# Kernel optimization log

Measured on AMD Instinct MI355X. Metric: run time of the kernel, lower is better.

The kernel has to match this reference:

```python
import jax, jax.numpy as jnp
import numpy as np

EPS = 1e-5

def layernorm(x, w, b):
    mu = jnp.mean(x, axis=-1, keepdims=True)
    xc = x - mu
    var = jnp.mean(xc * xc, axis=-1, keepdims=True)
    return xc * jax.lax.rsqrt(var + EPS) * w + b

def setup_inputs() -> dict:
    key = jax.random.key(0)
    ks = jax.random.split(key, 9)
    B, T, Nm, Nl = 8, 8, 1024, 64
    Vw, Tw, H, Dh = 1024, 2048, 8, 64
    inner = H * Dh  # 512
    s_q = 1.0 / np.sqrt(Tw)
    s_kv = 1.0 / np.sqrt(Vw)
    s_o = 1.0 / np.sqrt(inner)
    return {
        "x": jax.random.normal(ks[0], (B, T, Nm, Vw), jnp.float32),
        "latents": jax.random.normal(ks[1], (B, T, Nl, Tw), jnp.float32),
        "nm_w": jnp.ones((Vw,), jnp.float32),
        "nm_b": jnp.zeros((Vw,), jnp.float32),
        "nl_w": jnp.ones((Tw,), jnp.float32),
        "nl_b": jnp.zeros((Tw,), jnp.float32),
        "Wq": jax.random.normal(ks[2], (Tw, inner), jnp.float32) * s_q,
        "Wkv": jax.random.normal(ks[3], (Vw, 2 * inner), jnp.float32) * s_kv,
        "Wout": jax.random.normal(ks[4], (inner, Tw), jnp.float32) * s_o,
    }

def reference(x, latents, nm_w, nm_b, nl_w, nl_b, Wq, Wkv, Wout):
    H, Dh = 8, 64
    scale = Dh ** (-0.5)
    B, T, Nm, _ = x.shape
    Nl = latents.shape[2]
    xn = layernorm(x, nm_w, nm_b)          # (B,T,Nm,Vw)
    ln = layernorm(latents, nl_w, nl_b)    # (B,T,Nl,Tw)
    q = (ln @ Wq).reshape(B, T, Nl, H, Dh)           # b t i h d
    kv = xn @ Wkv                                     # (B,T,Nm,2*inner)
    k, v = jnp.split(kv, 2, axis=-1)
    k = k.reshape(B, T, Nm, H, Dh)                    # b t j h d
    v = v.reshape(B, T, Nm, H, Dh)
    sim = jnp.einsum('btihd,btjhd->bthij', q * scale, k)  # (B,T,H,Nl,Nm)
    attn = jax.nn.softmax(sim, axis=-1)
    out = jnp.einsum('bthij,btjhd->btihd', attn, v)       # (B,T,Nl,H,Dh)
    out = out.reshape(B, T, Nl, H * Dh)
    return out @ Wout                                     # (B,T,Nl,Tw)
```

## Files before the change

### kernel.cpp

```cpp
#include <hip/hip_runtime.h>

typedef __attribute__((ext_vector_type(8))) short bfrag8;
typedef __attribute__((ext_vector_type(4))) float f32x4;

typedef const unsigned int __attribute__((address_space(1)))* gas1_u32;
typedef unsigned int __attribute__((address_space(3)))* gas3_u32;

#define DEV __device__ __forceinline__

DEV unsigned short f2bf(float f) {
  unsigned int u = __builtin_bit_cast(unsigned int, f);
  u += 0x7fffu + ((u >> 16) & 1u);
  return (unsigned short)(u >> 16);
}

DEV void gload_lds16(const void* g, void* l) {
  __builtin_amdgcn_global_load_lds((gas1_u32)g, (gas3_u32)l, 16, 0, 0);
}

__global__ __launch_bounds__(256) void k_pre(
    const float* __restrict__ x, unsigned short* __restrict__ xb,
    float* __restrict__ mu, float* __restrict__ rstd,
    const float* __restrict__ lat, const float* __restrict__ nl_w,
    const float* __restrict__ nl_b, unsigned short* __restrict__ lnb,
    const float* __restrict__ Wq,   unsigned short* __restrict__ WqT,
    const float* __restrict__ Wkv,  unsigned short* __restrict__ WkvT,
    const float* __restrict__ Wout, unsigned short* __restrict__ WoutT,
    const float* __restrict__ nm_w, const float* __restrict__ nm_b,
    float* __restrict__ part)
{
  __shared__ float smem[32 * 33];
  const int bid = blockIdx.x, tid = threadIdx.x;
  const int wid = tid >> 6, lane = tid & 63;

  if (bid < 16384) {
    const int row = bid * 4 + wid;
    const float* base = x + (size_t)row * 1024;
    float4 v[4];
    #pragma unroll
    for (int i = 0; i < 4; ++i) v[i] = ((const float4*)base)[i * 64 + lane];
    float s = 0.f, q = 0.f;
    #pragma unroll
    for (int i = 0; i < 4; ++i) {
      s += v[i].x + v[i].y + v[i].z + v[i].w;
      q += v[i].x*v[i].x + v[i].y*v[i].y + v[i].z*v[i].z + v[i].w*v[i].w;
    }
    #pragma unroll
    for (int off = 32; off >= 1; off >>= 1) { s += __shfl_xor(s, off); q += __shfl_xor(q, off); }
    const float m  = s * (1.0f/1024.0f);
    const float var = q * (1.0f/1024.0f) - m * m;
    const float rs = rsqrtf(var + 1e-5f);
    if (lane == 0) { mu[row] = m; rstd[row] = rs; }
    unsigned short* ob = xb + (size_t)row * 1024;
    #pragma unroll
    for (int i = 0; i < 4; ++i) {
      ushort4 o;
      o.x = f2bf(v[i].x); o.y = f2bf(v[i].y); o.z = f2bf(v[i].z); o.w = f2bf(v[i].w);
      ((ushort4*)ob)[i * 64 + lane] = o;
    }
    return;
  }
  if (bid < 20480) {
    const int row = bid - 16384;
    const float* base = lat + (size_t)row * 2048;
    const float4 v0 = ((const float4*)base)[tid];
    const float4 v1 = ((const float4*)base)[256 + tid];
    float s = v0.x+v0.y+v0.z+v0.w + v1.x+v1.y+v1.z+v1.w;
    float q = v0.x*v0.x+v0.y*v0.y+v0.z*v0.z+v0.w*v0.w
            + v1.x*v1.x+v1.y*v1.y+v1.z*v1.z+v1.w*v1.w;
    #pragma unroll
    for (int off = 32; off >= 1; off >>= 1) { s += __shfl_xor(s, off); q += __shfl_xor(q, off); }
    if (lane == 0) { smem[wid] = s; smem[4 + wid] = q; }
    __syncthreads();
    s = smem[0] + smem[1] + smem[2] + smem[3];
    q = smem[4] + smem[5] + smem[6] + smem[7];
    const float m  = s * (1.0f/2048.0f);
    const float var = q * (1.0f/2048.0f) - m * m;
    const float rs = rsqrtf(var + 1e-5f);
    const float4 w0 = ((const float4*)nl_w)[tid], w1 = ((const float4*)nl_w)[256 + tid];
    const float4 b0 = ((const float4*)nl_b)[tid], b1 = ((const float4*)nl_b)[256 + tid];
    ushort4 o0, o1;
    o0.x = f2bf((v0.x - m) * rs * w0.x + b0.x);
    o0.y = f2bf((v0.y - m) * rs * w0.y + b0.y);
    o0.z = f2bf((v0.z - m) * rs * w0.z + b0.z);
    o0.w = f2bf((v0.w - m) * rs * w0.w + b0.w);
    o1.x = f2bf((v1.x - m) * rs * w1.x + b1.x);
    o1.y = f2bf((v1.y - m) * rs * w1.y + b1.y);
    o1.z = f2bf((v1.z - m) * rs * w1.z + b1.z);
    o1.w = f2bf((v1.w - m) * rs * w1.w + b1.w);
    ((ushort4*)(lnb + (size_t)row * 2048))[tid] = o0;
    ((ushort4*)(lnb + (size_t)row * 2048))[256 + tid] = o1;
    return;
  }
  if (bid < 23552) {
    int tb = bid - 20480;
    const float* src; unsigned short* dst; int Kd, N; const float* rsc; float sc;
    if (tb < 1024)      { src = Wq;   dst = WqT;   Kd = 2048; N = 512;  rsc = nullptr; sc = 0.125f; }
    else if (tb < 2048) { tb -= 1024; src = Wkv;  dst = WkvT;  Kd = 1024; N = 1024; rsc = nm_w;   sc = 1.0f; }
    else                { tb -= 2048; src = Wout; dst = WoutT; Kd = 512;  N = 2048; rsc = nullptr; sc = 1.0f; }
    float (*tile)[33] = (float(*)[33])smem;
    const int tx = tid & 31, ty = tid >> 5;
    const int ntiles = N >> 5;
    const int k0 = (tb / ntiles) << 5;
    const int n0 = (tb % ntiles) << 5;
    #pragma unroll
    for (int r = 0; r < 4; ++r) {
      const int kk = ty + r * 8;
      float v = src[(size_t)(k0 + kk) * N + n0 + tx] * sc;
      if (rsc) v *= rsc[k0 + kk];
      tile[kk][tx] = v;
    }
    __syncthreads();
    #pragma unroll
    for (int r = 0; r < 4; ++r) {
      const int nn = ty + r * 8;
      dst[(size_t)(n0 + nn) * Kd + k0 + tx] = f2bf(tile[tx][nn]);
    }
    return;
  }
  {
    const int cb = bid - 23552;
    const int kc = cb >> 2;
    const int n  = (cb & 3) * 256 + tid;
    float s1 = 0.f, s2 = 0.f;
    const int k0 = kc * 64;
    for (int k = k0; k < k0 + 64; ++k) {
      const float wv = Wkv[(size_t)k * 1024 + n];
      s1 += nm_w[k] * wv;
      s2 += nm_b[k] * wv;
    }
    part[(size_t)(kc * 2 + 0) * 1024 + n] = s1;
    part[(size_t)(kc * 2 + 1) * 1024 + n] = s2;
  }
}

__global__ __launch_bounds__(256) void k_c1c2_red(
    const float* __restrict__ part, float* __restrict__ c1, float* __restrict__ c2)
{
  const int n = blockIdx.x * 256 + threadIdx.x;
  float s1 = 0.f, s2 = 0.f;
  #pragma unroll
  for (int kc = 0; kc < 16; ++kc) {
    s1 += part[(size_t)(kc * 2 + 0) * 1024 + n];
    s2 += part[(size_t)(kc * 2 + 1) * 1024 + n];
  }
  c1[n] = s1; c2[n] = s2;
}

#define BAR8   __builtin_amdgcn_s_barrier()
#define GATE4  asm volatile("s_waitcnt vmcnt(4)\n\ts_barrier" ::: "memory")

__global__ __launch_bounds__(512, 2) void k_gemm8(
    const unsigned short* __restrict__ A,
    const unsigned short* __restrict__ Bt,
    unsigned short* __restrict__ C,
    const float* __restrict__ mu, const float* __restrict__ rstd,
    const float* __restrict__ c1, const float* __restrict__ c2)
{
  constexpr int NKT = 16;
  __shared__ __attribute__((aligned(16))) char lds[131072];

  int bid = blockIdx.x;
  { const int nwg = gridDim.x; const int q = nwg >> 3; bid = (bid & 7) * q + (bid >> 3); }
  const int mt = bid >> 2, nt = bid & 3;
  const int tid = threadIdx.x;
  const int wid = tid >> 6, lane = tid & 63;
  const int g = lane >> 4, c = lane & 15;
  const int wr = wid >> 2, wc = wid & 3;
  const int MO = wr * 128, NO = wc * 64;

  const unsigned short* gA = A + (size_t)mt * 256 * 1024;
  const unsigned short* gB = Bt + (size_t)nt * 256 * 1024;

  const f32x4 zz = {0.f, 0.f, 0.f, 0.f};
  f32x4 acc[8][4];
  #pragma unroll
  for (int m = 0; m < 8; ++m)
    #pragma unroll
    for (int n = 0; n < 4; ++n) acc[m][n] = zz;

  auto stageA = [&](int buf, int kk, int kt) {
    #pragma unroll
    for (int i = 0; i < 2; ++i) {
      const int o = (i * 512 + tid) * 16;
      const int row = o >> 6;
      const int ss = ((((o >> 4) & 3) - (row >> 1)) & 3);
      gload_lds16((const char*)(gA + (size_t)row * 1024 + kt * 64 + kk * 32) + ss * 16,
                  lds + buf * 32768 + kk * 16384 + o);
    }
  };
  auto stageB = [&](int buf, int kk, int kt) {
    #pragma unroll
    for (int i = 0; i < 2; ++i) {
      const int o = (i * 512 + tid) * 16;
      const int row = o >> 6;
      const int ss = ((((o >> 4) & 3) - (row >> 1)) & 3);
      gload_lds16((const char*)(gB + (size_t)row * 1024 + kt * 64 + kk * 32) + ss * 16,
                  lds + 65536 + buf * 32768 + kk * 16384 + o);
    }
  };
  auto rdA = [&](int buf, int kk, int m) -> bfrag8 {
    const int row = MO + m * 16 + c;
    return *(const bfrag8*)(lds + buf * 32768 + kk * 16384 + row * 64
                            + (((g + (row >> 1)) & 3) << 4));
  };
  auto rdB = [&](int buf, int kk, int n) -> bfrag8 {
    const int row = NO + n * 16 + c;
    return *(const bfrag8*)(lds + 65536 + buf * 32768 + kk * 16384 + row * 64
                            + (((g + (row >> 1)) & 3) << 4));
  };

  bfrag8 a[8], b0[4], b1[4];

  auto tile4 = [&](int buf, int sb, int ukt) {
    #pragma unroll
    for (int m = 0; m < 8; ++m) a[m] = rdA(buf, 0, m);
    #pragma unroll
    for (int n = 0; n < 4; ++n) b0[n] = rdB(buf, 0, n);
    stageA(sb, 0, ukt);
    __builtin_amdgcn_s_setprio(1);
    #pragma unroll
    for (int m = 0; m < 8; ++m) {
      acc[m][0] = __builtin_amdgcn_mfma_f32_16x16x32_bf16(a[m], b0[0], acc[m][0], 0, 0, 0);
      acc[m][1] = __builtin_amdgcn_mfma_f32_16x16x32_bf16(a[m], b0[1], acc[m][1], 0, 0, 0);
    }
    __builtin_amdgcn_s_setprio(0);
    GATE4;
    #pragma unroll
    for (int n = 0; n < 4; ++n) b1[n] = rdB(buf, 1, n);
    stageB(sb, 0, ukt);
    __builtin_amdgcn_s_setprio(1);
    #pragma unroll
    for (int m = 0; m < 8; ++m) {
      acc[m][2] = __builtin_amdgcn_mfma_f32_16x16x32_bf16(a[m], b0[2], acc[m][2], 0, 0, 0);
      acc[m][3] = __builtin_amdgcn_mfma_f32_16x16x32_bf16(a[m], b0[3], acc[m][3], 0, 0, 0);
    }
    __builtin_amdgcn_s_setprio(0);
    GATE4;
    #pragma unroll
    for (int m = 0; m < 8; ++m) a[m] = rdA(buf, 1, m);
    stageB(sb, 1, ukt);
    __builtin_amdgcn_s_setprio(1);
    #pragma unroll
    for (int m = 0; m < 8; ++m) {
      acc[m][0] = __builtin_amdgcn_mfma_f32_16x16x32_bf16(a[m], b1[0], acc[m][0], 0, 0, 0);
      acc[m][1] = __builtin_amdgcn_mfma_f32_16x16x32_bf16(a[m], b1[1], acc[m][1], 0, 0, 0);
    }
    __builtin_amdgcn_s_setprio(0);
    BAR8;
    stageA(sb, 1, ukt);
    __builtin_amdgcn_s_setprio(1);
    #pragma unroll
    for (int m = 0; m < 8; ++m) {
      acc[m][2] = __builtin_amdgcn_mfma_f32_16x16x32_bf16(a[m], b1[2], acc[m][2], 0, 0, 0);
      acc[m][3] = __builtin_amdgcn_mfma_f32_16x16x32_bf16(a[m], b1[3], acc[m][3], 0, 0, 0);
    }
    __builtin_amdgcn_s_setprio(0);
    GATE4;
  };

  stageA(0, 0, 0); stageB(0, 0, 0); stageB(0, 1, 0); stageA(0, 1, 0);
  GATE4;

  for (int t = 0; t < NKT; t += 2) {
    const int u2 = (t + 2 < NKT) ? t + 2 : 0;
    tile4(0, 1, t + 1);
    tile4(1, 0, u2);
  }
  asm volatile("s_waitcnt vmcnt(0)" ::: "memory");

  #pragma unroll
  for (int m = 0; m < 8; ++m) {
    #pragma unroll
    for (int j = 0; j < 4; ++j) {
      const size_t orow = (size_t)mt * 256 + MO + m * 16 + g * 4 + j;
      const float rs = rstd[orow], muv = mu[orow];
      #pragma unroll
      for (int n = 0; n < 4; ++n) {
        const int gcol = nt * 256 + NO + n * 16 + c;
        const float v = rs * (acc[m][n][j] - muv * c1[gcol]) + c2[gcol];
        C[orow * 1024 + gcol] = f2bf(v);
      }
    }
  }
}

template<int BM, int BN, int WM, int WN, int NT, int MODE>
__global__ __launch_bounds__(NT, 2) void k_gemm(
    const unsigned short* __restrict__ A, int lda,
    const unsigned short* __restrict__ Bt, int ldb,
    int K, int mtiles, int ntiles,
    void* __restrict__ Cout, int ldc)
{
  constexpr int BK = 64;
  constexpr int NW = NT / 64;
  constexpr int MF = (BM / WM) / 16;
  constexpr int NF = (BN / WN) / 16;
  constexpr int LA = (BM * BK) / (8 * NT);
  constexpr int LB = (BN * BK) / (8 * NT);
  static_assert(WM * WN == NW, "wave grid");
  static_assert(LA >= 1 && LB >= 1, "tile too small for NT");

  __shared__ __attribute__((aligned(16))) unsigned short As[2][BM * BK];
  __shared__ __attribute__((aligned(16))) unsigned short Bs[2][BN * BK];

  int bid = blockIdx.x;
  {
    const int nwg = gridDim.x;
    if ((nwg & 7) == 0) {
      const int q = nwg >> 3;
      bid = (bid & 7) * q + (bid >> 3);
    }
  }
  const int mt = bid / ntiles, nt = bid % ntiles;
  const int tid = threadIdx.x;
  const int wid = tid >> 6, lane = tid & 63;
  const int g = lane >> 4, c = lane & 15;
  const int wr = wid / WN, wc = wid % WN;
  const int MO = wr * (BM / WM), NO = wc * (BN / WN);

  const unsigned short* gA = A + (size_t)mt * BM * lda;
  const unsigned short* gB = Bt + (size_t)nt * BN * ldb;

  const f32x4 zz = {0.f, 0.f, 0.f, 0.f};
  f32x4 acc[MF][NF];
  #pragma unroll
  for (int m = 0; m < MF; ++m)
    #pragma unroll
    for (int n = 0; n < NF; ++n) acc[m][n] = zz;

  auto stage = [&](int buf, int kt) {
    #pragma unroll
    for (int i = 0; i < LA; ++i) {
      const int o = (i * NT + tid) * 16;
      const int row = o >> 7;
      const int sg = (((o >> 4) & 7) - row) & 7;
      gload_lds16((const char*)(gA + (size_t)row * lda + kt * BK) + sg * 16,
                  (char*)&As[buf][0] + o);
    }
    #pragma unroll
    for (int i = 0; i < LB; ++i) {
      const int o = (i * NT + tid) * 16;
      const int row = o >> 7;
      const int sg = (((o >> 4) & 7) - row) & 7;
      gload_lds16((const char*)(gB + (size_t)row * ldb + kt * BK) + sg * 16,
                  (char*)&Bs[buf][0] + o);
    }
  };

  auto compute = [&](int buf) {
    #pragma unroll
    for (int kk = 0; kk < 2; ++kk) {
      bfrag8 af[MF], bf[NF];
      #pragma unroll
      for (int m = 0; m < MF; ++m) {
        const int rw = MO + m * 16 + c;
        af[m] = *(const bfrag8*)((const char*)&As[buf][0] + rw * 128
                                 + (((kk * 4 + g + rw) & 7) << 4));
      }
      #pragma unroll
      for (int n = 0; n < NF; ++n) {
        const int rw = NO + n * 16 + c;
        bf[n] = *(const bfrag8*)((const char*)&Bs[buf][0] + rw * 128
                                 + (((kk * 4 + g + rw) & 7) << 4));
      }
      #pragma unroll
      for (int m = 0; m < MF; ++m)
        #pragma unroll
        for (int n = 0; n < NF; ++n)
          acc[m][n] = __builtin_amdgcn_mfma_f32_16x16x32_bf16(af[m], bf[n], acc[m][n], 0, 0, 0);
    }
  };

  const int nkt = K / BK;
  stage(0, 0);
  __syncthreads();
  for (int t = 0; t < nkt; t += 2) {
    if (t + 1 < nkt) stage(1, t + 1);
    compute(0);
    __syncthreads();
    if (t + 2 < nkt) stage(0, t + 2);
    if (t + 1 < nkt) compute(1);
    __syncthreads();
  }

  #pragma unroll
  for (int m = 0; m < MF; ++m) {
    #pragma unroll
    for (int j = 0; j < 4; ++j) {
      const size_t orow = (size_t)mt * BM + MO + m * 16 + g * 4 + j;
      #pragma unroll
      for (int n = 0; n < NF; ++n) {
        const int gcol = nt * BN + NO + n * 16 + c;
        const float v = acc[m][n][j];
        if constexpr (MODE == 2) ((float*)Cout)[orow * ldc + gcol] = v;
        else ((unsigned short*)Cout)[orow * ldc + gcol] = f2bf(v);
      }
    }
  }
}

__global__ __launch_bounds__(256) void k_attn(
    const unsigned short* __restrict__ q,
    const unsigned short* __restrict__ kv,
    unsigned short* __restrict__ ao)
{
  __shared__ __attribute__((aligned(16))) unsigned short Vt[64 * 64];
  const int bid = blockIdx.x;
  const int bt = bid >> 3, h = bid & 7;
  const int tid = threadIdx.x;
  const int wid = tid >> 6, lane = tid & 63;
  const int g = lane >> 4, c = lane & 15;

  const size_t qoff = ((size_t)bt * 64 + wid * 16 + c) * 512 + h * 64;
  const bfrag8 qf0 = *(const bfrag8*)(q + qoff + g * 8);
  const bfrag8 qf1 = *(const bfrag8*)(q + qoff + 32 + g * 8);

  const f32x4 zz = {0.f, 0.f, 0.f, 0.f};
  f32x4 o[4] = {zz, zz, zz, zz};
  float m_run = -1e30f, l_run = 0.f;

  const size_t kvbase = (size_t)bt * 1024 * 1024;
  const unsigned short* kbase = kv + kvbase + h * 64;
  const unsigned short* vbase = kv + kvbase + 512 + h * 64;

  for (int ch = 0; ch < 16; ++ch) {
    #pragma unroll
    for (int rr = 0; rr < 2; ++rr) {
      const int key = rr * 32 + (tid >> 3);
      const int d0 = (tid & 7) * 8;
      const bfrag8 vv = *(const bfrag8*)(vbase + (size_t)(ch * 64 + key) * 1024 + d0);
      #pragma unroll
      for (int j = 0; j < 8; ++j)
        Vt[(d0 + j) * 64 + (key ^ (j << 3))] = (unsigned short)vv[j];
    }
    __syncthreads();
    #pragma unroll
    for (int ks = 0; ks < 2; ++ks) {
      const int kb = ch * 64 + ks * 32;
      f32x4 s[2];
      #pragma unroll
      for (int t = 0; t < 2; ++t) {
        const int kr = ((c >> 2) << 3) + (t << 2) + (c & 3);
        const unsigned short* krow = kbase + (size_t)(kb + kr) * 1024;
        s[t] = zz;
        s[t] = __builtin_amdgcn_mfma_f32_16x16x32_bf16(*(const bfrag8*)(krow + g * 8),      qf0, s[t], 0, 0, 0);
        s[t] = __builtin_amdgcn_mfma_f32_16x16x32_bf16(*(const bfrag8*)(krow + 32 + g * 8), qf1, s[t], 0, 0, 0);
      }
      float pm = s[0][0];
      #pragma unroll
      for (int i = 1; i < 4; ++i) pm = fmaxf(pm, s[0][i]);
      #pragma unroll
      for (int i = 0; i < 4; ++i) pm = fmaxf(pm, s[1][i]);
      pm = fmaxf(pm, __shfl_xor(pm, 16));
      pm = fmaxf(pm, __shfl_xor(pm, 32));
      const float mn = fmaxf(m_run, pm);
      const float alpha = __expf(m_run - mn);
      float p[8];
      #pragma unroll
      for (int i = 0; i < 4; ++i) p[i]     = __expf(s[0][i] - mn);
      #pragma unroll
      for (int i = 0; i < 4; ++i) p[4 + i] = __expf(s[1][i] - mn);
      float ts = 0.f;
      #pragma unroll
      for (int i = 0; i < 8; ++i) ts += p[i];
      ts += __shfl_xor(ts, 16);
      ts += __shfl_xor(ts, 32);
      l_run = l_run * alpha + ts;
      m_run = mn;
      float ar[4];
      #pragma unroll
      for (int rj = 0; rj < 4; ++rj) ar[rj] = __shfl(alpha, g * 4 + rj);
      #pragma unroll
      for (int db = 0; db < 4; ++db)
        #pragma unroll
        for (int j = 0; j < 4; ++j) o[db][j] *= ar[j];
      bfrag8 pa;
      #pragma unroll
      for (int i = 0; i < 8; ++i) pa[i] = (short)f2bf(p[i]);
      #pragma unroll
      for (int db = 0; db < 4; ++db) {
        const int d = db * 16 + c;
        const bfrag8 vb = *(const bfrag8*)(Vt + d * 64 + ((ks * 32 + g * 8) ^ ((c & 7) << 3)));
        o[db] = __builtin_amdgcn_mfma_f32_16x16x32_bf16(pa, vb, o[db], 0, 0, 0);
      }
    }
    __syncthreads();
  }
  float lr[4];
  #pragma unroll
  for (int rj = 0; rj < 4; ++rj) lr[rj] = __shfl(l_run, g * 4 + rj);
  #pragma unroll
  for (int db = 0; db < 4; ++db)
    #pragma unroll
    for (int j = 0; j < 4; ++j) {
      const float val = o[db][j] / lr[j];
      ao[((size_t)bt * 64 + wid * 16 + g * 4 + j) * 512 + h * 64 + db * 16 + c] = f2bf(val);
    }
}

extern "C" void kernel_launch(void* const* d_in, const int* in_sizes, int n_in,
                              void* d_out, int out_size, void* d_ws, size_t ws_size,
                              hipStream_t stream)
{
  const float* x    = (const float*)d_in[0];
  const float* lat  = (const float*)d_in[1];
  const float* nm_w = (const float*)d_in[2];
  const float* nm_b = (const float*)d_in[3];
  const float* nl_w = (const float*)d_in[4];
  const float* nl_b = (const float*)d_in[5];
  const float* Wq   = (const float*)d_in[6];
  const float* Wkv  = (const float*)d_in[7];
  const float* Wout = (const float*)d_in[8];

  char* p = (char*)d_ws;
  auto take = [&](size_t bytes) { char* r = p; p += (bytes + 255) & ~(size_t)255; return r; };
  unsigned short* xb    = (unsigned short*)take(64ull * 1024 * 1024 * 2);
  unsigned short* kvb   = (unsigned short*)take(64ull * 1024 * 1024 * 2);
  unsigned short* lnb   = (unsigned short*)take(4096ull * 2048 * 2);
  unsigned short* qbuf  = (unsigned short*)take(4096ull * 512 * 2);
  unsigned short* aob   = (unsigned short*)take(4096ull * 512 * 2);
  unsigned short* WqT   = (unsigned short*)take(512ull * 2048 * 2);
  unsigned short* WkvT  = (unsigned short*)take(1024ull * 1024 * 2);
  unsigned short* WoutT = (unsigned short*)take(2048ull * 512 * 2);
  float* muv  = (float*)take(65536ull * 4);
  float* rsd  = (float*)take(65536ull * 4);
  float* c1   = (float*)take(1024 * 4);
  float* c2   = (float*)take(1024 * 4);
  float* part = (float*)take(32ull * 1024 * 4);
  if ((size_t)(p - (char*)d_ws) > ws_size) return;

  k_pre<<<dim3(23616), 256, 0, stream>>>(x, xb, muv, rsd,
                                         lat, nl_w, nl_b, lnb,
                                         Wq, WqT, Wkv, WkvT, Wout, WoutT,
                                         nm_w, nm_b, part);
  k_c1c2_red<<<dim3(4), 256, 0, stream>>>(part, c1, c2);

  k_gemm8<<<dim3(1024), 512, 0, stream>>>(xb, WkvT, kvb, muv, rsd, c1, c2);
  k_gemm<64, 128, 1, 4, 256, 1><<<dim3(256), 256, 0, stream>>>(
      lnb, 2048, WqT, 2048, 2048, 64, 4, qbuf, 512);

  k_attn<<<dim3(512), 256, 0, stream>>>(qbuf, kvb, aob);

  k_gemm<64, 128, 1, 4, 256, 2><<<dim3(1024), 256, 0, stream>>>(
      aob, 512, WoutT, 512, 512, 64, 16, d_out, 2048);
}
```

Measured before the change: 363.0 us.

## Merge KV and Q projection GEMMs into a single launch

The KV projection GEMM and the Q projection GEMM now run in one kernel launch. The first 1024 blocks do the KV GEMM as before, and the extra 128 blocks do the Q GEMM with a new 64x256 tile path using 512 threads and double-buffered LDS. This removes one launch and its tail/serialization, so the Q work can fill idle CUs during the KV GEMM's tail. The risk is that the Q blocks inherit the 512-thread, 128KB-LDS footprint, which may cap occupancy, and they form a long-K tail at the end of the grid.

New measurement: 356.0 us. Within noise of the previous version (-1.9%).

```diff
diff --git a/kernel.cpp b/kernel.cpp
--- a/kernel.cpp
+++ b/kernel.cpp
@@ -150,136 +150,229 @@
 #define BAR8   __builtin_amdgcn_s_barrier()
 #define GATE4  asm volatile("s_waitcnt vmcnt(4)\n\ts_barrier" ::: "memory")
 
-__global__ __launch_bounds__(512, 2) void k_gemm8(
+__global__ __launch_bounds__(512, 2) void k_mm(
     const unsigned short* __restrict__ A,
     const unsigned short* __restrict__ Bt,
     unsigned short* __restrict__ C,
     const float* __restrict__ mu, const float* __restrict__ rstd,
-    const float* __restrict__ c1, const float* __restrict__ c2)
+    const float* __restrict__ c1, const float* __restrict__ c2,
+    const unsigned short* __restrict__ Aq,
+    const unsigned short* __restrict__ Bq,
+    unsigned short* __restrict__ Cq)
 {
-  constexpr int NKT = 16;
   __shared__ __attribute__((aligned(16))) char lds[131072];
-
-  int bid = blockIdx.x;
-  { const int nwg = gridDim.x; const int q = nwg >> 3; bid = (bid & 7) * q + (bid >> 3); }
-  const int mt = bid >> 2, nt = bid & 3;
   const int tid = threadIdx.x;
   const int wid = tid >> 6, lane = tid & 63;
   const int g = lane >> 4, c = lane & 15;
-  const int wr = wid >> 2, wc = wid & 3;
-  const int MO = wr * 128, NO = wc * 64;
-
-  const unsigned short* gA = A + (size_t)mt * 256 * 1024;
-  const unsigned short* gB = Bt + (size_t)nt * 256 * 1024;
-
-  const f32x4 zz = {0.f, 0.f, 0.f, 0.f};
-  f32x4 acc[8][4];
-  #pragma unroll
-  for (int m = 0; m < 8; ++m)
-    #pragma unroll
-    for (int n = 0; n < 4; ++n) acc[m][n] = zz;
-
-  auto stageA = [&](int buf, int kk, int kt) {
-    #pragma unroll
-    for (int i = 0; i < 2; ++i) {
-      const int o = (i * 512 + tid) * 16;
-      const int row = o >> 6;
-      const int ss = ((((o >> 4) & 3) - (row >> 1)) & 3);
-      gload_lds16((const char*)(gA + (size_t)row * 1024 + kt * 64 + kk * 32) + ss * 16,
-                  lds + buf * 32768 + kk * 16384 + o);
-    }
-  };
-  auto stageB = [&](int buf, int kk, int kt) {
-    #pragma unroll
-    for (int i = 0; i < 2; ++i) {
-      const int o = (i * 512 + tid) * 16;
-      const int row = o >> 6;
-      const int ss = ((((o >> 4) & 3) - (row >> 1)) & 3);
-      gload_lds16((const char*)(gB + (size_t)row * 1024 + kt * 64 + kk * 32) + ss * 16,
-                  lds + 65536 + buf * 32768 + kk * 16384 + o);
-    }
-  };
-  auto rdA = [&](int buf, int kk, int m) -> bfrag8 {
-    const int row = MO + m * 16 + c;
-    return *(const bfrag8*)(lds + buf * 32768 + kk * 16384 + row * 64
-                            + (((g + (row >> 1)) & 3) << 4));
-  };
-  auto rdB = [&](int buf, int kk, int n) -> bfrag8 {
-    const int row = NO + n * 16 + c;
-    return *(const bfrag8*)(lds + 65536 + buf * 32768 + kk * 16384 + row * 64
-                            + (((g + (row >> 1)) & 3) << 4));
-  };
-
-  bfrag8 a[8], b0[4], b1[4];
-
-  auto tile4 = [&](int buf, int sb, int ukt) {
-    #pragma unroll
-    for (int m = 0; m < 8; ++m) a[m] = rdA(buf, 0, m);
-    #pragma unroll
-    for (int n = 0; n < 4; ++n) b0[n] = rdB(buf, 0, n);
-    stageA(sb, 0, ukt);
-    __builtin_amdgcn_s_setprio(1);
+
+  if (blockIdx.x < 1024) {
+    constexpr int NKT = 16;
+    int bid = blockIdx.x;
+    bid = (bid & 7) * 128 + (bid >> 3);
+    const int mt = bid >> 2, nt = bid & 3;
+    const int wr = wid >> 2, wc = wid & 3;
+    const int MO = wr * 128, NO = wc * 64;
+
+    const unsigned short* gA = A + (size_t)mt * 256 * 1024;
+    const unsigned short* gB = Bt + (size_t)nt * 256 * 1024;
+
+    const f32x4 zz = {0.f, 0.f, 0.f, 0.f};
+    f32x4 acc[8][4];
+    #pragma unroll
+    for (int m = 0; m < 8; ++m)
+      #pragma unroll
+      for (int n = 0; n < 4; ++n) acc[m][n] = zz;
+
+    auto stageA = [&](int buf, int kk, int kt) {
+      #pragma unroll
+      for (int i = 0; i < 2; ++i) {
+        const int o = (i * 512 + tid) * 16;
+        const int row = o >> 6;
+        const int ss = ((((o >> 4) & 3) - (row >> 1)) & 3);
+        gload_lds16((const char*)(gA + (size_t)row * 1024 + kt * 64 + kk * 32) + ss * 16,
+                    lds + buf * 32768 + kk * 16384 + o);
+      }
+    };
+    auto stageB = [&](int buf, int kk, int kt) {
+      #pragma unroll
+      for (int i = 0; i < 2; ++i) {
+        const int o = (i * 512 + tid) * 16;
+        const int row = o >> 6;
+        const int ss = ((((o >> 4) & 3) - (row >> 1)) & 3);
+        gload_lds16((const char*)(gB + (size_t)row * 1024 + kt * 64 + kk * 32) + ss * 16,
+                    lds + 65536 + buf * 32768 + kk * 16384 + o);
+      }
+    };
+    auto rdA = [&](int buf, int kk, int m) -> bfrag8 {
+      const int row = MO + m * 16 + c;
+      return *(const bfrag8*)(lds + buf * 32768 + kk * 16384 + row * 64
+                              + (((g + (row >> 1)) & 3) << 4));
+    };
+    auto rdB = [&](int buf, int kk, int n) -> bfrag8 {
+      const int row = NO + n * 16 + c;
+      return *(const bfrag8*)(lds + 65536 + buf * 32768 + kk * 16384 + row * 64
+                              + (((g + (row >> 1)) & 3) << 4));
+    };
+
+    bfrag8 a[8], b0[4], b1[4];
+
+    auto tile4 = [&](int buf, int sb, int ukt) {
+      #pragma unroll
+      for (int m = 0; m < 8; ++m) a[m] = rdA(buf, 0, m);
+      #pragma unroll
+      for (int n = 0; n < 4; ++n) b0[n] = rdB(buf, 0, n);
+      stageA(sb, 0, ukt);
+      __builtin_amdgcn_s_setprio(1);
+      #pragma unroll
+      for (int m = 0; m < 8; ++m) {
+        acc[m][0] = __builtin_amdgcn_mfma_f32_16x16x32_bf16(a[m], b0[0], acc[m][0], 0, 0, 0);
+        acc[m][1] = __builtin_amdgcn_mfma_f32_16x16x32_bf16(a[m], b0[1], acc[m][1], 0, 0, 0);
+      }
+      __builtin_amdgcn_s_setprio(0);
+      GATE4;
+      #pragma unroll
+      for (int n = 0; n < 4; ++n) b1[n] = rdB(buf, 1, n);
+      stageB(sb, 0, ukt);
+      __builtin_amdgcn_s_setprio(1);
+      #pragma unroll
+      for (int m = 0; m < 8; ++m) {
+        acc[m][2] = __builtin_amdgcn_mfma_f32_16x16x32_bf16(a[m], b0[2], acc[m][2], 0, 0, 0);
+        acc[m][3] = __builtin_amdgcn_mfma_f32_16x16x32_bf16(a[m], b0[3], acc[m][3], 0, 0, 0);
+      }
+      __builtin_amdgcn_s_setprio(0);
+      GATE4;
+      #pragma unroll
+      for (int m = 0; m < 8; ++m) a[m] = rdA(buf, 1, m);
+      stageB(sb, 1, ukt);
+      __builtin_amdgcn_s_setprio(1);
+      #pragma unroll
+      for (int m = 0; m < 8; ++m) {
+        acc[m][0] = __builtin_amdgcn_mfma_f32_16x16x32_bf16(a[m], b1[0], acc[m][0], 0, 0, 0);
+        acc[m][1] = __builtin_amdgcn_mfma_f32_16x16x32_bf16(a[m], b1[1], acc[m][1], 0, 0, 0);
+      }
+      __builtin_amdgcn_s_setprio(0);
+      BAR8;
+      stageA(sb, 1, ukt);
+      __builtin_amdgcn_s_setprio(1);
+      #pragma unroll
+      for (int m = 0; m < 8; ++m) {
+        acc[m][2] = __builtin_amdgcn_mfma_f32_16x16x32_bf16(a[m], b1[2], acc[m][2], 0, 0, 0);
+        acc[m][3] = __builtin_amdgcn_mfma_f32_16x16x32_bf16(a[m], b1[3], acc[m][3], 0, 0, 0);
+      }
+      __builtin_amdgcn_s_setprio(0);
+      GATE4;
+    };
+
+    stageA(0, 0, 0); stageB(0, 0, 0); stageB(0, 1, 0); stageA(0, 1, 0);
+    GATE4;
+
+    for (int t = 0; t < NKT; t += 2) {
+      const int u2 = (t + 2 < NKT) ? t + 2 : 0;
+      tile4(0, 1, t + 1);
+      tile4(1, 0, u2);
+    }
+    asm volatile("s_waitcnt vmcnt(0)" ::: "memory");
+
     #pragma unroll
     for (int m = 0; m < 8; ++m) {
-      acc[m][0] = __builtin_amdgcn_mfma_f32_16x16x32_bf16(a[m], b0[0], acc[m][0], 0, 0, 0);
-      acc[m][1] = __builtin_amdgcn_mfma_f32_16x16x32_bf16(a[m], b0[1], acc[m][1], 0, 0, 0);
-    }
-    __builtin_amdgcn_s_setprio(0);
-    GATE4;
-    #pragma unroll
-    for (int n = 0; n < 4; ++n) b1[n] = rdB(buf, 1, n);
-    stageB(sb, 0, ukt);
-    __builtin_amdgcn_s_setprio(1);
-    #pragma unroll
-    for (int m = 0; m < 8; ++m) {
-      acc[m][2] = __builtin_amdgcn_mfma_f32_16x16x32_bf16(a[m], b0[2], acc[m][2], 0, 0, 0);
-      acc[m][3] = __builtin_amdgcn_mfma_f32_16x16x32_bf16(a[m], b0[3], acc[m][3], 0, 0, 0);
-    }
-    __builtin_amdgcn_s_setprio(0);
-    GATE4;
-    #pragma unroll
-    for (int m = 0; m < 8; ++m) a[m] = rdA(buf, 1, m);
-    stageB(sb, 1, ukt);
-    __builtin_amdgcn_s_setprio(1);
-    #pragma unroll
-    for (int m = 0; m < 8; ++m) {
-      acc[m][0] = __builtin_amdgcn_mfma_f32_16x16x32_bf16(a[m], b1[0], acc[m][0], 0, 0, 0);
-      acc[m][1] = __builtin_amdgcn_mfma_f32_16x16x32_bf16(a[m], b1[1], acc[m][1], 0, 0, 0);
-    }
-    __builtin_amdgcn_s_setprio(0);
-    BAR8;
-    stageA(sb, 1, ukt);
-    __builtin_amdgcn_s_setprio(1);
-    #pragma unroll
-    for (int m = 0; m < 8; ++m) {
-      acc[m][2] = __builtin_amdgcn_mfma_f32_16x16x32_bf16(a[m], b1[2], acc[m][2], 0, 0, 0);
-      acc[m][3] = __builtin_amdgcn_mfma_f32_16x16x32_bf16(a[m], b1[3], acc[m][3], 0, 0, 0);
-    }
-    __builtin_amdgcn_s_setprio(0);
-    GATE4;
-  };
-
-  stageA(0, 0, 0); stageB(0, 0, 0); stageB(0, 1, 0); stageA(0, 1, 0);
-  GATE4;
-
-  for (int t = 0; t < NKT; t += 2) {
-    const int u2 = (t + 2 < NKT) ? t + 2 : 0;
-    tile4(0, 1, t + 1);
-    tile4(1, 0, u2);
-  }
-  asm volatile("s_waitcnt vmcnt(0)" ::: "memory");
-
-  #pragma unroll
-  for (int m = 0; m < 8; ++m) {
-    #pragma unroll
-    for (int j = 0; j < 4; ++j) {
-      const size_t orow = (size_t)mt * 256 + MO + m * 16 + g * 4 + j;
-      const float rs = rstd[orow], muv = mu[orow];
-      #pragma unroll
-      for (int n = 0; n < 4; ++n) {
-        const int gcol = nt * 256 + NO + n * 16 + c;
-        const float v = rs * (acc[m][n][j] - muv * c1[gcol]) + c2[gcol];
-        C[orow * 1024 + gcol] = f2bf(v);
+      #pragma unroll
+      for (int j = 0; j < 4; ++j) {
+        const size_t orow = (size_t)mt * 256 + MO + m * 16 + g * 4 + j;
+        const float rs = rstd[orow], muv = mu[orow];
+        #pragma unroll
+        for (int n = 0; n < 4; ++n) {
+          const int gcol = nt * 256 + NO + n * 16 + c;
+          const float v = rs * (acc[m][n][j] - muv * c1[gcol]) + c2[gcol];
+          C[orow * 1024 + gcol] = f2bf(v);
+        }
+      }
+    }
+    return;
+  }
+
+  {
+    constexpr int BK = 64, MF = 4, NF = 2;
+    int lb = blockIdx.x - 1024;
+    lb = (lb & 7) * 16 + (lb >> 3);
+    const int mt = lb >> 1, nt = lb & 1;
+    const int NO = (wid & 7) * 32;
+    const int MO = 0;
+
+    const unsigned short* gA = Aq + (size_t)mt * 64 * 2048;
+    const unsigned short* gB = Bq + (size_t)nt * 256 * 2048;
+    auto asb = [&](int buf) { return lds + buf * 8192; };
+    auto bsb = [&](int buf) { return lds + 16384 + buf * 32768; };
+
+    const f32x4 zz = {0.f, 0.f, 0.f, 0.f};
+    f32x4 acc[MF][NF];
+    #pragma unroll
+    for (int m = 0; m < MF; ++m)
+      #pragma unroll
+      for (int n = 0; n < NF; ++n) acc[m][n] = zz;
+
+    auto stage = [&](int buf, int kt) {
+      {
+        const int o = tid * 16;
+        const int row = o >> 7;
+        const int sg = (((o >> 4) & 7) - row) & 7;
+        gload_lds16((const char*)(gA + (size_t)row * 2048 + kt * BK) + sg * 16,
+                    asb(buf) + o);
+      }
+      #pragma unroll
+      for (int i = 0; i < 4; ++i) {
+        const int o = (i * 512 + tid) * 16;
+        const int row = o >> 7;
+        const int sg = (((o >> 4) & 7) - row) & 7;
+        gload_lds16((const char*)(gB + (size_t)row * 2048 + kt * BK) + sg * 16,
+                    bsb(buf) + o);
+      }
+    };
+    auto compute = [&](int buf) {
+      #pragma unroll
+      for (int kk = 0; kk < 2; ++kk) {
+        bfrag8 af[MF], bf[NF];
+        #pragma unroll
+        for (int m = 0; m < MF; ++m) {
+          const int rw = MO + m * 16 + c;
+          af[m] = *(const bfrag8*)((const char*)asb(buf) + rw * 128
+                                   + (((kk * 4 + g + rw) & 7) << 4));
+        }
+        #pragma unroll
+        for (int n = 0; n < NF; ++n) {
+          const int rw = NO + n * 16 + c;
+          bf[n] = *(const bfrag8*)((const char*)bsb(buf) + rw * 128
+                                   + (((kk * 4 + g + rw) & 7) << 4));
+        }
+        #pragma unroll
+        for (int m = 0; m < MF; ++m)
+          #pragma unroll
+          for (int n = 0; n < NF; ++n)
+            acc[m][n] = __builtin_amdgcn_mfma_f32_16x16x32_bf16(af[m], bf[n], acc[m][n], 0, 0, 0);
+      }
+    };
+
+    const int nkt = 2048 / BK;
+    stage(0, 0);
+    __syncthreads();
+    for (int t = 0; t < nkt; t += 2) {
+      if (t + 1 < nkt) stage(1, t + 1);
+      compute(0);
+      __syncthreads();
+      if (t + 2 < nkt) stage(0, t + 2);
+      if (t + 1 < nkt) compute(1);
+      __syncthreads();
+    }
+
+    #pragma unroll
+    for (int m = 0; m < MF; ++m) {
+      #pragma unroll
+      for (int j = 0; j < 4; ++j) {
+        const size_t orow = (size_t)mt * 64 + MO + m * 16 + g * 4 + j;
+        #pragma unroll
+        for (int n = 0; n < NF; ++n) {
+          const int gcol = nt * 256 + NO + n * 16 + c;
+          Cq[orow * 512 + gcol] = f2bf(acc[m][n][j]);
+        }
       }
     }
   }
@@ -536,9 +629,8 @@
                                          nm_w, nm_b, part);
   k_c1c2_red<<<dim3(4), 256, 0, stream>>>(part, c1, c2);
 
-  k_gemm8<<<dim3(1024), 512, 0, stream>>>(xb, WkvT, kvb, muv, rsd, c1, c2);
-  k_gemm<64, 128, 1, 4, 256, 1><<<dim3(256), 256, 0, stream>>>(
-      lnb, 2048, WqT, 2048, 2048, 64, 4, qbuf, 512);
+  k_mm<<<dim3(1152), 512, 0, stream>>>(xb, WkvT, kvb, muv, rsd, c1, c2,
+                                       lnb, WqT, qbuf);
 
   k_attn<<<dim3(512), 256, 0, stream>>>(qbuf, kvb, aob);
 
```
